# Kernel optimization log

Measured on AMD Instinct MI355X. Metric: run time of the kernel, lower is better.

Reference implementation:

```python
import jax, jax.numpy as jnp
import numpy as np

B, T, D, H, O = 64, 2048, 256, 256, 256


def setup_inputs() -> dict:
    key = jax.random.key(0)
    ks = jax.random.split(key, 4)
    s_d = float(1.0 / np.sqrt(D))
    s_h = float(1.0 / np.sqrt(H))
    return {
        "x": jax.random.normal(ks[0], (B, T, D), jnp.float32),
        "c0": jnp.zeros((B, H), jnp.float32),
        "h0": jnp.zeros((B, H), jnp.float32),
        "Wih": jax.random.normal(ks[1], (D, 4 * H), jnp.float32) * s_d,
        "Whh": jax.random.normal(ks[2], (H, 4 * H), jnp.float32) * s_h,
        "bh": jnp.zeros((4 * H,), jnp.float32),
        "Wout": jax.random.normal(ks[3], (H, O), jnp.float32) * s_h,
        "bout": jnp.zeros((O,), jnp.float32),
    }


def reference(x, c0, h0, Wih, Whh, bh, Wout, bout):
    # Teacher-forcing OneToManyRNN: LSTM cell + Dense projection each step.
    # Gate order (flax LSTMCell): i, f, g, o.
    def step(carry, xt):
        c, h = carry
        gates = xt @ Wih + h @ Whh + bh  # [B, 4H]
        i, f, g, o = jnp.split(gates, 4, axis=-1)
        i = jax.nn.sigmoid(i)
        f = jax.nn.sigmoid(f)
        g = jnp.tanh(g)
        o = jax.nn.sigmoid(o)
        c_new = f * c + i * g
        h_new = o * jnp.tanh(c_new)
        y = h_new @ Wout + bout  # dense_out projection
        return (c_new, h_new), y

    xs = jnp.swapaxes(x, 0, 1)  # [T, B, D]
    _, ys = jax.lax.scan(step, (c0, h0), xs)
    return jnp.swapaxes(ys, 0, 1)  # [B, T, O] (stacked per-step outputs)
```

## Files before the change

### kernel.cpp

```cpp
#include <hip/hip_runtime.h>
#include <hip/hip_fp16.h>
#include <cstdint>
#include <cstddef>

typedef _Float16 half_t;
typedef _Float16 half2_t __attribute__((ext_vector_type(2)));
typedef _Float16 half8_t __attribute__((ext_vector_type(8)));
typedef float    f32x4   __attribute__((ext_vector_type(4)));

#define T_FULL  2048
#define T_CH    512
#define N_CHUNK 4
#define B_SZ    64
#define H_SZ    256
#define G4      1024
#define CH_M    (B_SZ * T_CH)

#define KP_RF   48
#define KP_LDS  7
#define KP_STR  9

static constexpr size_t OFF_XW   = 0;
static constexpr size_t OFF_H    = OFF_XW   + (size_t)CH_M * G4 * 2;
static constexpr size_t OFF_WIH  = OFF_H    + (size_t)CH_M * H_SZ * 2;
static constexpr size_t OFF_WOUT = OFF_WIH  + (size_t)G4 * 256 * 2;
static constexpr size_t OFF_WRF  = OFF_WOUT + (size_t)256 * 256 * 2;
static constexpr size_t OFF_WLDS = OFF_WRF  + (size_t)2 * KP_RF * 1024 * 4;
static constexpr size_t OFF_WSTR = OFF_WLDS + (size_t)2 * KP_LDS * 256 * 16;
static constexpr size_t OFF_SC   = OFF_WSTR + (size_t)2 * KP_STR * 256 * 16;
static constexpr size_t OFF_SH   = OFF_SC   + (size_t)B_SZ * H_SZ * 4;

__device__ __forceinline__ unsigned int packh2(float a, float b) {
    half2_t h; h.x = (half_t)a; h.y = (half_t)b;
    return __builtin_bit_cast(unsigned int, h);
}

__device__ __forceinline__ float dot2f(unsigned int hp, unsigned int wp, float acc) {
#if __has_builtin(__builtin_amdgcn_fdot2)
    return __builtin_amdgcn_fdot2(__builtin_bit_cast(half2_t, hp),
                                  __builtin_bit_cast(half2_t, wp), acc, false);
#else
    half2_t h = __builtin_bit_cast(half2_t, hp);
    half2_t w = __builtin_bit_cast(half2_t, wp);
    return fmaf((float)h.y, (float)w.y, fmaf((float)h.x, (float)w.x, acc));
#endif
}

__device__ __forceinline__ unsigned int rlane(unsigned int v, int lane) {
    return (unsigned int)__builtin_amdgcn_readlane((int)v, lane);
}

__device__ __forceinline__ float sigm(float x)  { return 1.0f / (1.0f + __expf(-x)); }
__device__ __forceinline__ float tanh_(float x) { return 1.0f - 2.0f / (__expf(2.0f * x) + 1.0f); }

static constexpr int PACK_TOTAL = 262144 + 65536 + 2 * KP_RF * 1024
                                + 2 * KP_LDS * 256 * 4 + 2 * KP_STR * 256 * 4
                                + 16384 + 8192;

__global__ __launch_bounds__(256) void pack_kernel(
    const float* __restrict__ Wih, const float* __restrict__ Whh,
    const float* __restrict__ Wout, const float* __restrict__ c0,
    const float* __restrict__ h0,
    half_t* __restrict__ wih_t, half_t* __restrict__ wout_t,
    unsigned int* __restrict__ whh_rf, unsigned int* __restrict__ whh_lds,
    unsigned int* __restrict__ whh_str,
    float* __restrict__ state_c, unsigned int* __restrict__ state_h)
{
    const int stride = gridDim.x * blockDim.x;
    for (int idx = blockIdx.x * blockDim.x + threadIdx.x; idx < PACK_TOTAL; idx += stride) {
        int r = idx;
        if (r < 262144) {
            int n = r >> 8, k = r & 255;
            wih_t[r] = (half_t)Wih[k * 1024 + n];
            continue;
        }
        r -= 262144;
        if (r < 65536) {
            int n = r >> 8, k = r & 255;
            wout_t[r] = (half_t)Wout[k * 256 + n];
            continue;
        }
        r -= 65536;
        if (r < 2 * KP_RF * 1024) {
            int col = r & 1023, q2 = r >> 10;
            int hh = q2 / KP_RF, pl = q2 % KP_RF;
            int k0 = 2 * (hh * 64 + pl);
            whh_rf[r] = packh2(Whh[k0 * 1024 + col], Whh[(k0 + 1) * 1024 + col]);
            continue;
        }
        r -= 2 * KP_RF * 1024;
        if (r < 2 * KP_LDS * 256 * 4) {
            int j = r & 3, e = (r >> 2) & 255, rest = r >> 10;
            int ql = rest % KP_LDS, hh = rest / KP_LDS;
            int k0 = 2 * (hh * 64 + KP_RF + ql);
            int col = j * 256 + e;
            whh_lds[r] = packh2(Whh[k0 * 1024 + col], Whh[(k0 + 1) * 1024 + col]);
            continue;
        }
        r -= 2 * KP_LDS * 256 * 4;
        if (r < 2 * KP_STR * 256 * 4) {
            int j = r & 3, e = (r >> 2) & 255, rest = r >> 10;
            int sl = rest % KP_STR, hh = rest / KP_STR;
            int k0 = 2 * (hh * 64 + KP_RF + KP_LDS + sl);
            int col = j * 256 + e;
            whh_str[r] = packh2(Whh[k0 * 1024 + col], Whh[(k0 + 1) * 1024 + col]);
            continue;
        }
        r -= 2 * KP_STR * 256 * 4;
        if (r < 16384) { state_c[r] = c0[r]; continue; }
        r -= 16384;
        state_h[r] = packh2(h0[2 * r], h0[2 * r + 1]);
    }
}

template<int AMODE, int CMODE>
__global__ __launch_bounds__(256) void gemm16(
    const void* __restrict__ Ap, const half_t* __restrict__ Bt,
    void* __restrict__ Cp, const float* __restrict__ bias, int chunk0)
{
    __shared__ half_t Als[128][40];
    __shared__ half_t Bls[128][40];
    const int tid  = threadIdx.x;
    const int lane = tid & 63, wid = tid >> 6;
    const int wr = wid >> 1, wc = wid & 1;
    const int m0 = blockIdx.x * 128, n0 = blockIdx.y * 128;

    f32x4 acc[4][4] = {};

    for (int kc = 0; kc < 8; ++kc) {
        __syncthreads();
        if (AMODE == 1) {
            const float* A = (const float*)Ap;
            #pragma unroll
            for (int i = 0; i < 4; ++i) {
                int l = tid + i * 256;
                int row = l >> 3, kq = l & 7;
                int m = m0 + row;
                int arow = ((m >> 9) << 11) + chunk0 + (m & 511);
                f32x4 v = *(const f32x4*)(A + (size_t)arow * 256 + kc * 32 + kq * 4);
                uint2 pk;
                pk.x = packh2(v.x, v.y);
                pk.y = packh2(v.z, v.w);
                *reinterpret_cast<uint2*>(&Als[row][kq * 4]) = pk;
            }
        } else {
            const half_t* A = (const half_t*)Ap;
            #pragma unroll
            for (int i = 0; i < 2; ++i) {
                int l = tid + i * 256;
                int row = l >> 2, ko = l & 3;
                half8_t v = *(const half8_t*)(A + (size_t)(m0 + row) * 256 + kc * 32 + ko * 8);
                *reinterpret_cast<half8_t*>(&Als[row][ko * 8]) = v;
            }
        }
        #pragma unroll
        for (int i = 0; i < 2; ++i) {
            int l = tid + i * 256;
            int row = l >> 2, ko = l & 3;
            half8_t v = *(const half8_t*)(Bt + (size_t)(n0 + row) * 256 + kc * 32 + ko * 8);
            *reinterpret_cast<half8_t*>(&Bls[row][ko * 8]) = v;
        }
        __syncthreads();

        half8_t af[4], bf[4];
        #pragma unroll
        for (int mi = 0; mi < 4; ++mi)
            af[mi] = *reinterpret_cast<const half8_t*>(&Als[wr * 64 + mi * 16 + (lane & 15)][(lane >> 4) * 8]);
        #pragma unroll
        for (int ni = 0; ni < 4; ++ni)
            bf[ni] = *reinterpret_cast<const half8_t*>(&Bls[wc * 64 + ni * 16 + (lane & 15)][(lane >> 4) * 8]);
        #pragma unroll
        for (int mi = 0; mi < 4; ++mi)
            #pragma unroll
            for (int ni = 0; ni < 4; ++ni)
                acc[mi][ni] = __builtin_amdgcn_mfma_f32_16x16x32_f16(af[mi], bf[ni], acc[mi][ni], 0, 0, 0);
    }

    #pragma unroll
    for (int mi = 0; mi < 4; ++mi) {
        #pragma unroll
        for (int ni = 0; ni < 4; ++ni) {
            #pragma unroll
            for (int reg = 0; reg < 4; ++reg) {
                int row = m0 + wr * 64 + mi * 16 + (lane >> 4) * 4 + reg;
                int col = n0 + wc * 64 + ni * 16 + (lane & 15);
                float v = acc[mi][ni][reg] + bias[col];
                if (CMODE == 0) {
                    ((half_t*)Cp)[(size_t)row * 1024 + ((col & 255) << 2) + (col >> 8)] = (half_t)v;
                } else {
                    int crow = ((row >> 9) << 11) + chunk0 + (row & 511);
                    ((float*)Cp)[(size_t)crow * 256 + col] = v;
                }
            }
        }
    }
}

__global__ __launch_bounds__(512, 2) void rnn_kernel(
    const unsigned int* __restrict__ whh_rf,
    const uint4* __restrict__ whh_lds,
    const uint4* __restrict__ whh_str,
    const half_t* __restrict__ xw,
    half_t* __restrict__ h_out,
    float* __restrict__ state_c,
    unsigned int* __restrict__ state_h)
{
    __shared__ uint4  lds_w[2 * KP_LDS * 256];
    __shared__ float4 gbuf[256];
    __shared__ unsigned int hbuf[128];

    const int t    = threadIdx.x;
    const int e    = t & 255;
    const int hh   = t >> 8;
    const int lane = t & 63;
    const int b    = blockIdx.x;

    for (int i = t; i < 2 * KP_LDS * 256; i += 512) lds_w[i] = whh_lds[i];
    if (t < 128) hbuf[t] = state_h[b * 128 + t];
    float c = (hh == 0) ? state_c[b * 256 + e] : 0.0f;

    unsigned int wreg[KP_RF][4];
    {
        const unsigned int* wrp = whh_rf + hh * (KP_RF * 1024) + e;
        #pragma unroll
        for (int pl = 0; pl < KP_RF; ++pl)
            #pragma unroll
            for (int j = 0; j < 4; ++j)
                wreg[pl][j] = wrp[pl * 1024 + j * 256];
    }
    __syncthreads();

    const half_t* xwp = xw + (size_t)b * T_CH * 1024 + e * 4;
    half_t* hop = h_out + (size_t)b * T_CH * 256 + e;
    const uint4* strp = whh_str + hh * (KP_STR * 256) + e;
    const uint4* ldp  = lds_w + hh * (KP_LDS * 256) + e;

    for (int step = 0; step < T_CH; ++step) {
        unsigned int hv = hbuf[hh * 64 + lane];

        uint2 xv = {0, 0};
        if (hh == 0) xv = *(const uint2*)xwp;
        uint4 sq[KP_STR];
        #pragma unroll
        for (int sl = 0; sl < KP_STR; ++sl) sq[sl] = strp[sl * 256];

        float a0 = 0.f, a1 = 0.f, a2 = 0.f, a3 = 0.f;

        #pragma unroll
        for (int pl = 0; pl < KP_RF; ++pl) {
            unsigned int s = rlane(hv, pl);
            a0 = dot2f(s, wreg[pl][0], a0);
            a1 = dot2f(s, wreg[pl][1], a1);
            a2 = dot2f(s, wreg[pl][2], a2);
            a3 = dot2f(s, wreg[pl][3], a3);
        }
        #pragma unroll
        for (int sl = 0; sl < KP_STR; ++sl) {
            unsigned int s = rlane(hv, KP_RF + KP_LDS + sl);
            a0 = dot2f(s, sq[sl].x, a0);
            a1 = dot2f(s, sq[sl].y, a1);
            a2 = dot2f(s, sq[sl].z, a2);
            a3 = dot2f(s, sq[sl].w, a3);
        }
        #pragma unroll
        for (int ql = 0; ql < KP_LDS; ++ql) {
            uint4 q = ldp[ql * 256];
            unsigned int s = rlane(hv, KP_RF + ql);
            a0 = dot2f(s, q.x, a0);
            a1 = dot2f(s, q.y, a1);
            a2 = dot2f(s, q.z, a2);
            a3 = dot2f(s, q.w, a3);
        }

        if (hh) {
            float4 p; p.x = a0; p.y = a1; p.z = a2; p.w = a3;
            gbuf[e] = p;
        }
        __syncthreads();

        if (hh == 0) {
            float4 p = gbuf[e];
            half2_t x0 = __builtin_bit_cast(half2_t, xv.x);
            half2_t x1 = __builtin_bit_cast(half2_t, xv.y);
            a0 += p.x + (float)x0.x;
            a1 += p.y + (float)x0.y;
            a2 += p.z + (float)x1.x;
            a3 += p.w + (float)x1.y;
            float ig = sigm(a0), fg = sigm(a1), gg = tanh_(a2), og = sigm(a3);
            c = fg * c + ig * gg;
            float hn = og * tanh_(c);
            half_t h16 = (half_t)hn;
            reinterpret_cast<half_t*>(hbuf)[e] = h16;
            *hop = h16;
        }
        xwp += 1024;
        hop += 256;
        __syncthreads();
    }

    if (hh == 0) state_c[b * 256 + e] = c;
    if (t < 128) state_h[b * 128 + t] = hbuf[t];
}

extern "C" void kernel_launch(void* const* d_in, const int* in_sizes, int n_in,
                              void* d_out, int out_size, void* d_ws, size_t ws_size,
                              hipStream_t stream) {
    const float* x    = (const float*)d_in[0];
    const float* c0   = (const float*)d_in[1];
    const float* h0   = (const float*)d_in[2];
    const float* Wih  = (const float*)d_in[3];
    const float* Whh  = (const float*)d_in[4];
    const float* bh   = (const float*)d_in[5];
    const float* Wout = (const float*)d_in[6];
    const float* bout = (const float*)d_in[7];

    char* ws = (char*)d_ws;
    half_t* xw             = (half_t*)(ws + OFF_XW);
    half_t* h_chunk        = (half_t*)(ws + OFF_H);
    half_t* wih_t          = (half_t*)(ws + OFF_WIH);
    half_t* wout_t         = (half_t*)(ws + OFF_WOUT);
    unsigned int* whh_rf   = (unsigned int*)(ws + OFF_WRF);
    unsigned int* whh_lds  = (unsigned int*)(ws + OFF_WLDS);
    unsigned int* whh_str  = (unsigned int*)(ws + OFF_WSTR);
    float* state_c         = (float*)(ws + OFF_SC);
    unsigned int* state_h  = (unsigned int*)(ws + OFF_SH);

    pack_kernel<<<512, 256, 0, stream>>>(Wih, Whh, Wout, c0, h0,
                                         wih_t, wout_t, whh_rf, whh_lds, whh_str,
                                         state_c, state_h);

    for (int ch = 0; ch < N_CHUNK; ++ch) {
        int chunk0 = ch * T_CH;
        gemm16<1, 0><<<dim3(CH_M / 128, G4 / 128), 256, 0, stream>>>(
            (const void*)x, wih_t, (void*)xw, bh, chunk0);
        rnn_kernel<<<B_SZ, 512, 0, stream>>>(whh_rf, (const uint4*)whh_lds,
                                             (const uint4*)whh_str, xw, h_chunk,
                                             state_c, state_h);
        gemm16<0, 1><<<dim3(CH_M / 128, H_SZ / 128), 256, 0, stream>>>(
            (const void*)h_chunk, wout_t, d_out, bout, chunk0);
    }
    (void)in_sizes; (void)n_in; (void)out_size; (void)ws_size;
}
```

Baseline: 4.092 ms.

## Rebalance Whh split toward LDS, pin register weights, interleave loads with dots

Moves two k-pairs of the recurrent weights from per-step global streaming to LDS and repacks the register-resident weights as 16-byte vectors held in named variables pinned with empty asm, so the compiler keeps them in VGPRs. The step loop is split into two halves, each issuing its global and LDS loads before the register-weight dot products to hide load latency. The h output store moves after the second barrier. It adds LDS usage and depends on the compiler honouring the register pinning without spilling.

```diff
diff --git a/kernel.cpp b/kernel.cpp
--- a/kernel.cpp
+++ b/kernel.cpp
@@ -7,6 +7,7 @@
 typedef _Float16 half2_t __attribute__((ext_vector_type(2)));
 typedef _Float16 half8_t __attribute__((ext_vector_type(8)));
 typedef float    f32x4   __attribute__((ext_vector_type(4)));
+typedef unsigned int uint4v __attribute__((ext_vector_type(4)));
 
 #define T_FULL  2048
 #define T_CH    512
@@ -17,15 +18,15 @@
 #define CH_M    (B_SZ * T_CH)
 
 #define KP_RF   48
-#define KP_LDS  7
-#define KP_STR  9
+#define KP_LDS  9
+#define KP_STR  7
 
 static constexpr size_t OFF_XW   = 0;
 static constexpr size_t OFF_H    = OFF_XW   + (size_t)CH_M * G4 * 2;
 static constexpr size_t OFF_WIH  = OFF_H    + (size_t)CH_M * H_SZ * 2;
 static constexpr size_t OFF_WOUT = OFF_WIH  + (size_t)G4 * 256 * 2;
 static constexpr size_t OFF_WRF  = OFF_WOUT + (size_t)256 * 256 * 2;
-static constexpr size_t OFF_WLDS = OFF_WRF  + (size_t)2 * KP_RF * 1024 * 4;
+static constexpr size_t OFF_WLDS = OFF_WRF  + (size_t)2 * KP_RF * 256 * 16;
 static constexpr size_t OFF_WSTR = OFF_WLDS + (size_t)2 * KP_LDS * 256 * 16;
 static constexpr size_t OFF_SC   = OFF_WSTR + (size_t)2 * KP_STR * 256 * 16;
 static constexpr size_t OFF_SH   = OFF_SC   + (size_t)B_SZ * H_SZ * 4;
@@ -53,8 +54,10 @@
 __device__ __forceinline__ float sigm(float x)  { return 1.0f / (1.0f + __expf(-x)); }
 __device__ __forceinline__ float tanh_(float x) { return 1.0f - 2.0f / (__expf(2.0f * x) + 1.0f); }
 
-static constexpr int PACK_TOTAL = 262144 + 65536 + 2 * KP_RF * 1024
-                                + 2 * KP_LDS * 256 * 4 + 2 * KP_STR * 256 * 4
+static constexpr int PACK_TOTAL = 262144 + 65536
+                                + 2 * KP_RF  * 256 * 4
+                                + 2 * KP_LDS * 256 * 4
+                                + 2 * KP_STR * 256 * 4
                                 + 16384 + 8192;
 
 __global__ __launch_bounds__(256) void pack_kernel(
@@ -81,17 +84,18 @@
             continue;
         }
         r -= 65536;
-        if (r < 2 * KP_RF * 1024) {
-            int col = r & 1023, q2 = r >> 10;
-            int hh = q2 / KP_RF, pl = q2 % KP_RF;
+        if (r < 2 * KP_RF * 256 * 4) {
+            int j = r & 3, e = (r >> 2) & 255, q = r >> 10;
+            int pl = q % KP_RF, hh = q / KP_RF;
             int k0 = 2 * (hh * 64 + pl);
+            int col = j * 256 + e;
             whh_rf[r] = packh2(Whh[k0 * 1024 + col], Whh[(k0 + 1) * 1024 + col]);
             continue;
         }
-        r -= 2 * KP_RF * 1024;
+        r -= 2 * KP_RF * 256 * 4;
         if (r < 2 * KP_LDS * 256 * 4) {
-            int j = r & 3, e = (r >> 2) & 255, rest = r >> 10;
-            int ql = rest % KP_LDS, hh = rest / KP_LDS;
+            int j = r & 3, e = (r >> 2) & 255, q = r >> 10;
+            int ql = q % KP_LDS, hh = q / KP_LDS;
             int k0 = 2 * (hh * 64 + KP_RF + ql);
             int col = j * 256 + e;
             whh_lds[r] = packh2(Whh[k0 * 1024 + col], Whh[(k0 + 1) * 1024 + col]);
@@ -99,8 +103,8 @@
         }
         r -= 2 * KP_LDS * 256 * 4;
         if (r < 2 * KP_STR * 256 * 4) {
-            int j = r & 3, e = (r >> 2) & 255, rest = r >> 10;
-            int sl = rest % KP_STR, hh = rest / KP_STR;
+            int j = r & 3, e = (r >> 2) & 255, q = r >> 10;
+            int sl = q % KP_STR, hh = q / KP_STR;
             int k0 = 2 * (hh * 64 + KP_RF + KP_LDS + sl);
             int col = j * 256 + e;
             whh_str[r] = packh2(Whh[k0 * 1024 + col], Whh[(k0 + 1) * 1024 + col]);
@@ -196,17 +200,35 @@
     }
 }
 
+#define W_A(F) F(0) F(1) F(2) F(3) F(4) F(5) F(6) F(7) F(8) F(9) F(10) F(11) \
+               F(12) F(13) F(14) F(15) F(16) F(17) F(18) F(19) F(20) F(21) F(22) F(23)
+#define W_B(F) F(24) F(25) F(26) F(27) F(28) F(29) F(30) F(31) F(32) F(33) F(34) F(35) \
+               F(36) F(37) F(38) F(39) F(40) F(41) F(42) F(43) F(44) F(45) F(46) F(47)
+#define W_ALL(F) W_A(F) W_B(F)
+
+#define LDW(i)  uint4v w##i = wq[(i) * 256];
+#define PINW(i) asm volatile("" : "+v"(w##i));
+#define DOTW(i) { unsigned int s = rlane(hv, (i)); \
+    a0 = dot2f(s, w##i.x, a0); a1 = dot2f(s, w##i.y, a1); \
+    a2 = dot2f(s, w##i.z, a2); a3 = dot2f(s, w##i.w, a3); }
+#define DOTQ(i, q) { unsigned int s = rlane(hv, KP_RF + (i)); \
+    a0 = dot2f(s, (q).x, a0); a1 = dot2f(s, (q).y, a1); \
+    a2 = dot2f(s, (q).z, a2); a3 = dot2f(s, (q).w, a3); }
+#define DOTS(i, q) { unsigned int s = rlane(hv, KP_RF + KP_LDS + (i)); \
+    a0 = dot2f(s, (q).x, a0); a1 = dot2f(s, (q).y, a1); \
+    a2 = dot2f(s, (q).z, a2); a3 = dot2f(s, (q).w, a3); }
+
 __global__ __launch_bounds__(512, 2) void rnn_kernel(
-    const unsigned int* __restrict__ whh_rf,
-    const uint4* __restrict__ whh_lds,
-    const uint4* __restrict__ whh_str,
+    const uint4v* __restrict__ whh_rf,
+    const uint4v* __restrict__ whh_ldsrc,
+    const uint4v* __restrict__ whh_str,
     const half_t* __restrict__ xw,
     half_t* __restrict__ h_out,
     float* __restrict__ state_c,
     unsigned int* __restrict__ state_h)
 {
-    __shared__ uint4  lds_w[2 * KP_LDS * 256];
-    __shared__ float4 gbuf[256];
+    __shared__ uint4v lds_w[2 * KP_LDS * 256];
+    __shared__ f32x4  gbuf[256];
     __shared__ unsigned int hbuf[128];
 
     const int t    = threadIdx.x;
@@ -215,87 +237,75 @@
     const int lane = t & 63;
     const int b    = blockIdx.x;
 
-    for (int i = t; i < 2 * KP_LDS * 256; i += 512) lds_w[i] = whh_lds[i];
+    for (int i = t; i < 2 * KP_LDS * 256; i += 512) lds_w[i] = whh_ldsrc[i];
     if (t < 128) hbuf[t] = state_h[b * 128 + t];
     float c = (hh == 0) ? state_c[b * 256 + e] : 0.0f;
 
-    unsigned int wreg[KP_RF][4];
-    {
-        const unsigned int* wrp = whh_rf + hh * (KP_RF * 1024) + e;
-        #pragma unroll
-        for (int pl = 0; pl < KP_RF; ++pl)
-            #pragma unroll
-            for (int j = 0; j < 4; ++j)
-                wreg[pl][j] = wrp[pl * 1024 + j * 256];
-    }
+    const uint4v* wq = whh_rf + (size_t)hh * (KP_RF * 256) + e;
+    W_ALL(LDW)
+    W_ALL(PINW)
     __syncthreads();
 
     const half_t* xwp = xw + (size_t)b * T_CH * 1024 + e * 4;
     half_t* hop = h_out + (size_t)b * T_CH * 256 + e;
-    const uint4* strp = whh_str + hh * (KP_STR * 256) + e;
-    const uint4* ldp  = lds_w + hh * (KP_LDS * 256) + e;
+    const uint4v* strp = whh_str + hh * (KP_STR * 256) + e;
+    const uint4v* ldp  = lds_w + hh * (KP_LDS * 256) + e;
 
     for (int step = 0; step < T_CH; ++step) {
         unsigned int hv = hbuf[hh * 64 + lane];
 
-        uint2 xv = {0, 0};
+        uint2 xv; xv.x = 0; xv.y = 0;
         if (hh == 0) xv = *(const uint2*)xwp;
-        uint4 sq[KP_STR];
-        #pragma unroll
-        for (int sl = 0; sl < KP_STR; ++sl) sq[sl] = strp[sl * 256];
 
         float a0 = 0.f, a1 = 0.f, a2 = 0.f, a3 = 0.f;
 
-        #pragma unroll
-        for (int pl = 0; pl < KP_RF; ++pl) {
-            unsigned int s = rlane(hv, pl);
-            a0 = dot2f(s, wreg[pl][0], a0);
-            a1 = dot2f(s, wreg[pl][1], a1);
-            a2 = dot2f(s, wreg[pl][2], a2);
-            a3 = dot2f(s, wreg[pl][3], a3);
-        }
-        #pragma unroll
-        for (int sl = 0; sl < KP_STR; ++sl) {
-            unsigned int s = rlane(hv, KP_RF + KP_LDS + sl);
-            a0 = dot2f(s, sq[sl].x, a0);
-            a1 = dot2f(s, sq[sl].y, a1);
-            a2 = dot2f(s, sq[sl].z, a2);
-            a3 = dot2f(s, sq[sl].w, a3);
-        }
-        #pragma unroll
-        for (int ql = 0; ql < KP_LDS; ++ql) {
-            uint4 q = ldp[ql * 256];
-            unsigned int s = rlane(hv, KP_RF + ql);
-            a0 = dot2f(s, q.x, a0);
-            a1 = dot2f(s, q.y, a1);
-            a2 = dot2f(s, q.z, a2);
-            a3 = dot2f(s, q.w, a3);
+        {
+            uint4v t0 = strp[0],   t1 = strp[256],  t2 = strp[512],  t3 = strp[768];
+            uint4v q0 = ldp[0],    q1 = ldp[256],   q2 = ldp[512],   q3 = ldp[768];
+
+            W_A(DOTW)
+
+            DOTQ(0, q0) DOTQ(1, q1) DOTQ(2, q2) DOTQ(3, q3)
+            DOTS(0, t0) DOTS(1, t1) DOTS(2, t2) DOTS(3, t3)
+        }
+
+        {
+            uint4v t4 = strp[1024], t5 = strp[1280], t6 = strp[1536];
+            uint4v q4 = ldp[1024],  q5 = ldp[1280],  q6 = ldp[1536], q7 = ldp[1792];
+            uint4v q8 = ldp[2048];
+
+            W_B(DOTW)
+
+            DOTQ(4, q4) DOTQ(5, q5) DOTQ(6, q6) DOTQ(7, q7) DOTQ(8, q8)
+            DOTS(4, t4) DOTS(5, t5) DOTS(6, t6)
         }
 
         if (hh) {
-            float4 p; p.x = a0; p.y = a1; p.z = a2; p.w = a3;
+            f32x4 p; p[0] = a0; p[1] = a1; p[2] = a2; p[3] = a3;
             gbuf[e] = p;
         }
         __syncthreads();
 
+        half_t h16 = (half_t)0.f;
         if (hh == 0) {
-            float4 p = gbuf[e];
+            f32x4 p = gbuf[e];
             half2_t x0 = __builtin_bit_cast(half2_t, xv.x);
             half2_t x1 = __builtin_bit_cast(half2_t, xv.y);
-            a0 += p.x + (float)x0.x;
-            a1 += p.y + (float)x0.y;
-            a2 += p.z + (float)x1.x;
-            a3 += p.w + (float)x1.y;
+            a0 += p[0] + (float)x0.x;
+            a1 += p[1] + (float)x0.y;
+            a2 += p[2] + (float)x1.x;
+            a3 += p[3] + (float)x1.y;
             float ig = sigm(a0), fg = sigm(a1), gg = tanh_(a2), og = sigm(a3);
             c = fg * c + ig * gg;
             float hn = og * tanh_(c);
-            half_t h16 = (half_t)hn;
+            h16 = (half_t)hn;
             reinterpret_cast<half_t*>(hbuf)[e] = h16;
-            *hop = h16;
         }
         xwp += 1024;
+        __syncthreads();
+
+        if (hh == 0) *hop = h16;
         hop += 256;
-        __syncthreads();
     }
 
     if (hh == 0) state_c[b * 256 + e] = c;
@@ -333,9 +343,10 @@
         int chunk0 = ch * T_CH;
         gemm16<1, 0><<<dim3(CH_M / 128, G4 / 128), 256, 0, stream>>>(
             (const void*)x, wih_t, (void*)xw, bh, chunk0);
-        rnn_kernel<<<B_SZ, 512, 0, stream>>>(whh_rf, (const uint4*)whh_lds,
-                                             (const uint4*)whh_str, xw, h_chunk,
-                                             state_c, state_h);
+        rnn_kernel<<<B_SZ, 512, 0, stream>>>((const uint4v*)(ws + OFF_WRF),
+                                             (const uint4v*)(ws + OFF_WLDS),
+                                             (const uint4v*)(ws + OFF_WSTR),
+                                             xw, h_chunk, state_c, state_h);
         gemm16<0, 1><<<dim3(CH_M / 128, H_SZ / 128), 256, 0, stream>>>(
             (const void*)h_chunk, wout_t, d_out, bout, chunk0);
     }
```

After: 4.158 ms. Within noise of the previous version (+1.6%).

## Compute recurrent Whh matvec with MFMA instead of fdot2 readlane broadcast

Applied to the files above, without the earlier changes.

Replaces the per-thread fdot2 recurrent matvec, which broadcast h with readlane, with 16x16x32 f16 MFMA instructions. Only row 0 of the A operand is non-zero, so most of each MFMA's work is discarded. Whh is repacked into an MFMA B-fragment layout and split three ways: half the K tiles stay resident in registers, a quarter sit in LDS, and a quarter are reloaded from global/L2 every step. The aim is to cut the VALU and readlane cost per timestep. In exchange it wastes most of the MFMA throughput, adds per-step global loads, and adds an extra barrier before the h store.

```diff
diff --git a/kernel.cpp b/kernel.cpp
--- a/kernel.cpp
+++ b/kernel.cpp
@@ -7,6 +7,7 @@
 typedef _Float16 half2_t __attribute__((ext_vector_type(2)));
 typedef _Float16 half8_t __attribute__((ext_vector_type(8)));
 typedef float    f32x4   __attribute__((ext_vector_type(4)));
+typedef unsigned int uint4v __attribute__((ext_vector_type(4)));
 
 #define T_FULL  2048
 #define T_CH    512
@@ -16,18 +17,12 @@
 #define G4      1024
 #define CH_M    (B_SZ * T_CH)
 
-#define KP_RF   48
-#define KP_LDS  7
-#define KP_STR  9
-
 static constexpr size_t OFF_XW   = 0;
 static constexpr size_t OFF_H    = OFF_XW   + (size_t)CH_M * G4 * 2;
 static constexpr size_t OFF_WIH  = OFF_H    + (size_t)CH_M * H_SZ * 2;
 static constexpr size_t OFF_WOUT = OFF_WIH  + (size_t)G4 * 256 * 2;
-static constexpr size_t OFF_WRF  = OFF_WOUT + (size_t)256 * 256 * 2;
-static constexpr size_t OFF_WLDS = OFF_WRF  + (size_t)2 * KP_RF * 1024 * 4;
-static constexpr size_t OFF_WSTR = OFF_WLDS + (size_t)2 * KP_LDS * 256 * 16;
-static constexpr size_t OFF_SC   = OFF_WSTR + (size_t)2 * KP_STR * 256 * 16;
+static constexpr size_t OFF_WMF  = OFF_WOUT + (size_t)256 * 256 * 2;
+static constexpr size_t OFF_SC   = OFF_WMF  + (size_t)8 * 64 * 64 * 16;
 static constexpr size_t OFF_SH   = OFF_SC   + (size_t)B_SZ * H_SZ * 4;
 
 __device__ __forceinline__ unsigned int packh2(float a, float b) {
@@ -35,35 +30,17 @@
     return __builtin_bit_cast(unsigned int, h);
 }
 
-__device__ __forceinline__ float dot2f(unsigned int hp, unsigned int wp, float acc) {
-#if __has_builtin(__builtin_amdgcn_fdot2)
-    return __builtin_amdgcn_fdot2(__builtin_bit_cast(half2_t, hp),
-                                  __builtin_bit_cast(half2_t, wp), acc, false);
-#else
-    half2_t h = __builtin_bit_cast(half2_t, hp);
-    half2_t w = __builtin_bit_cast(half2_t, wp);
-    return fmaf((float)h.y, (float)w.y, fmaf((float)h.x, (float)w.x, acc));
-#endif
-}
-
-__device__ __forceinline__ unsigned int rlane(unsigned int v, int lane) {
-    return (unsigned int)__builtin_amdgcn_readlane((int)v, lane);
-}
-
 __device__ __forceinline__ float sigm(float x)  { return 1.0f / (1.0f + __expf(-x)); }
 __device__ __forceinline__ float tanh_(float x) { return 1.0f - 2.0f / (__expf(2.0f * x) + 1.0f); }
 
-static constexpr int PACK_TOTAL = 262144 + 65536 + 2 * KP_RF * 1024
-                                + 2 * KP_LDS * 256 * 4 + 2 * KP_STR * 256 * 4
-                                + 16384 + 8192;
+static constexpr int PACK_TOTAL = 262144 + 65536 + 131072 + 16384 + 8192;
 
 __global__ __launch_bounds__(256) void pack_kernel(
     const float* __restrict__ Wih, const float* __restrict__ Whh,
     const float* __restrict__ Wout, const float* __restrict__ c0,
     const float* __restrict__ h0,
     half_t* __restrict__ wih_t, half_t* __restrict__ wout_t,
-    unsigned int* __restrict__ whh_rf, unsigned int* __restrict__ whh_lds,
-    unsigned int* __restrict__ whh_str,
+    unsigned int* __restrict__ whh_mf,
     float* __restrict__ state_c, unsigned int* __restrict__ state_h)
 {
     const int stride = gridDim.x * blockDim.x;
@@ -81,32 +58,17 @@
             continue;
         }
         r -= 65536;
-        if (r < 2 * KP_RF * 1024) {
-            int col = r & 1023, q2 = r >> 10;
-            int hh = q2 / KP_RF, pl = q2 % KP_RF;
-            int k0 = 2 * (hh * 64 + pl);
-            whh_rf[r] = packh2(Whh[k0 * 1024 + col], Whh[(k0 + 1) * 1024 + col]);
+        if (r < 131072) {
+            int j    = r & 3;
+            int lane = (r >> 2) & 63;
+            int nt   = (r >> 8) & 63;
+            int kt   = r >> 14;
+            int k0 = kt * 32 + ((lane >> 4) << 3) + 2 * j;
+            int n  = nt * 16 + (lane & 15);
+            whh_mf[r] = packh2(Whh[k0 * 1024 + n], Whh[(k0 + 1) * 1024 + n]);
             continue;
         }
-        r -= 2 * KP_RF * 1024;
-        if (r < 2 * KP_LDS * 256 * 4) {
-            int j = r & 3, e = (r >> 2) & 255, rest = r >> 10;
-            int ql = rest % KP_LDS, hh = rest / KP_LDS;
-            int k0 = 2 * (hh * 64 + KP_RF + ql);
-            int col = j * 256 + e;
-            whh_lds[r] = packh2(Whh[k0 * 1024 + col], Whh[(k0 + 1) * 1024 + col]);
-            continue;
-        }
-        r -= 2 * KP_LDS * 256 * 4;
-        if (r < 2 * KP_STR * 256 * 4) {
-            int j = r & 3, e = (r >> 2) & 255, rest = r >> 10;
-            int sl = rest % KP_STR, hh = rest / KP_STR;
-            int k0 = 2 * (hh * 64 + KP_RF + KP_LDS + sl);
-            int col = j * 256 + e;
-            whh_str[r] = packh2(Whh[k0 * 1024 + col], Whh[(k0 + 1) * 1024 + col]);
-            continue;
-        }
-        r -= 2 * KP_STR * 256 * 4;
+        r -= 131072;
         if (r < 16384) { state_c[r] = c0[r]; continue; }
         r -= 16384;
         state_h[r] = packh2(h0[2 * r], h0[2 * r + 1]);
@@ -196,109 +158,96 @@
     }
 }
 
-__global__ __launch_bounds__(512, 2) void rnn_kernel(
-    const unsigned int* __restrict__ whh_rf,
-    const uint4* __restrict__ whh_lds,
-    const uint4* __restrict__ whh_str,
+__global__ __launch_bounds__(512) void rnn_kernel(
+    const uint4v* __restrict__ whh_mf,
     const half_t* __restrict__ xw,
     half_t* __restrict__ h_out,
     float* __restrict__ state_c,
     unsigned int* __restrict__ state_h)
 {
-    __shared__ uint4  lds_w[2 * KP_LDS * 256];
-    __shared__ float4 gbuf[256];
+    __shared__ uint4v lds_b[2 * 4096];
+    __shared__ float  gbuf[1024];
     __shared__ unsigned int hbuf[128];
 
     const int t    = threadIdx.x;
+    const int lane = t & 63;
+    const int w    = t >> 6;
     const int e    = t & 255;
-    const int hh   = t >> 8;
-    const int lane = t & 63;
     const int b    = blockIdx.x;
 
-    for (int i = t; i < 2 * KP_LDS * 256; i += 512) lds_w[i] = whh_lds[i];
+    for (int i = t; i < 8192; i += 512) lds_b[i] = whh_mf[4 * 4096 + i];
     if (t < 128) hbuf[t] = state_h[b * 128 + t];
-    float c = (hh == 0) ? state_c[b * 256 + e] : 0.0f;
-
-    unsigned int wreg[KP_RF][4];
-    {
-        const unsigned int* wrp = whh_rf + hh * (KP_RF * 1024) + e;
-        #pragma unroll
-        for (int pl = 0; pl < KP_RF; ++pl)
-            #pragma unroll
-            for (int j = 0; j < 4; ++j)
-                wreg[pl][j] = wrp[pl * 1024 + j * 256];
-    }
+    float c = (t < 256) ? state_c[b * 256 + e] : 0.0f;
+
+    const half8_t* mf8 = (const half8_t*)whh_mf;
+    half8_t Bres[4][8];
+    #pragma unroll
+    for (int r = 0; r < 4; ++r)
+        #pragma unroll
+        for (int ntl = 0; ntl < 8; ++ntl)
+            Bres[r][ntl] = mf8[(r * 64 + w * 8 + ntl) * 64 + lane];
     __syncthreads();
 
     const half_t* xwp = xw + (size_t)b * T_CH * 1024 + e * 4;
     half_t* hop = h_out + (size_t)b * T_CH * 256 + e;
-    const uint4* strp = whh_str + hh * (KP_STR * 256) + e;
-    const uint4* ldp  = lds_w + hh * (KP_LDS * 256) + e;
-
+    const half_t* hbh = (const half_t*)hbuf;
+
+    #pragma unroll 1
     for (int step = 0; step < T_CH; ++step) {
-        unsigned int hv = hbuf[hh * 64 + lane];
-
-        uint2 xv = {0, 0};
-        if (hh == 0) xv = *(const uint2*)xwp;
-        uint4 sq[KP_STR];
-        #pragma unroll
-        for (int sl = 0; sl < KP_STR; ++sl) sq[sl] = strp[sl * 256];
-
-        float a0 = 0.f, a1 = 0.f, a2 = 0.f, a3 = 0.f;
-
-        #pragma unroll
-        for (int pl = 0; pl < KP_RF; ++pl) {
-            unsigned int s = rlane(hv, pl);
-            a0 = dot2f(s, wreg[pl][0], a0);
-            a1 = dot2f(s, wreg[pl][1], a1);
-            a2 = dot2f(s, wreg[pl][2], a2);
-            a3 = dot2f(s, wreg[pl][3], a3);
-        }
-        #pragma unroll
-        for (int sl = 0; sl < KP_STR; ++sl) {
-            unsigned int s = rlane(hv, KP_RF + KP_LDS + sl);
-            a0 = dot2f(s, sq[sl].x, a0);
-            a1 = dot2f(s, sq[sl].y, a1);
-            a2 = dot2f(s, sq[sl].z, a2);
-            a3 = dot2f(s, sq[sl].w, a3);
-        }
-        #pragma unroll
-        for (int ql = 0; ql < KP_LDS; ++ql) {
-            uint4 q = ldp[ql * 256];
-            unsigned int s = rlane(hv, KP_RF + ql);
-            a0 = dot2f(s, q.x, a0);
-            a1 = dot2f(s, q.y, a1);
-            a2 = dot2f(s, q.z, a2);
-            a3 = dot2f(s, q.w, a3);
-        }
-
-        if (hh) {
-            float4 p; p.x = a0; p.y = a1; p.z = a2; p.w = a3;
-            gbuf[e] = p;
-        }
-        __syncthreads();
-
-        if (hh == 0) {
-            float4 p = gbuf[e];
+        uint2 xv; xv.x = 0; xv.y = 0;
+        if (t < 256) xv = *(const uint2*)xwp;
+
+        half8_t a[8];
+        #pragma unroll
+        for (int kt = 0; kt < 8; ++kt) {
+            half8_t v = {};
+            if ((lane & 15) == 0)
+                v = *(const half8_t*)(hbh + kt * 32 + (lane >> 4) * 8);
+            a[kt] = v;
+        }
+
+        #pragma unroll
+        for (int ntl = 0; ntl < 8; ++ntl) {
+            const int nt = w * 8 + ntl;
+            half8_t l4 = *(const half8_t*)&lds_b[0 * 4096 + nt * 64 + lane];
+            half8_t l5 = *(const half8_t*)&lds_b[1 * 4096 + nt * 64 + lane];
+            half8_t g6 = mf8[(6 * 64 + nt) * 64 + lane];
+            half8_t g7 = mf8[(7 * 64 + nt) * 64 + lane];
+            f32x4 cc = {};
+            cc = __builtin_amdgcn_mfma_f32_16x16x32_f16(a[0], Bres[0][ntl], cc, 0, 0, 0);
+            cc = __builtin_amdgcn_mfma_f32_16x16x32_f16(a[1], Bres[1][ntl], cc, 0, 0, 0);
+            cc = __builtin_amdgcn_mfma_f32_16x16x32_f16(a[2], Bres[2][ntl], cc, 0, 0, 0);
+            cc = __builtin_amdgcn_mfma_f32_16x16x32_f16(a[3], Bres[3][ntl], cc, 0, 0, 0);
+            cc = __builtin_amdgcn_mfma_f32_16x16x32_f16(a[4], l4, cc, 0, 0, 0);
+            cc = __builtin_amdgcn_mfma_f32_16x16x32_f16(a[5], l5, cc, 0, 0, 0);
+            cc = __builtin_amdgcn_mfma_f32_16x16x32_f16(a[6], g6, cc, 0, 0, 0);
+            cc = __builtin_amdgcn_mfma_f32_16x16x32_f16(a[7], g7, cc, 0, 0, 0);
+            if (lane < 16) gbuf[nt * 16 + lane] = cc[0];
+        }
+        __syncthreads();
+
+        half_t h16 = (half_t)0.f;
+        if (t < 256) {
             half2_t x0 = __builtin_bit_cast(half2_t, xv.x);
             half2_t x1 = __builtin_bit_cast(half2_t, xv.y);
-            a0 += p.x + (float)x0.x;
-            a1 += p.y + (float)x0.y;
-            a2 += p.z + (float)x1.x;
-            a3 += p.w + (float)x1.y;
+            float a0 = gbuf[e]       + (float)x0.x;
+            float a1 = gbuf[256 + e] + (float)x0.y;
+            float a2 = gbuf[512 + e] + (float)x1.x;
+            float a3 = gbuf[768 + e] + (float)x1.y;
             float ig = sigm(a0), fg = sigm(a1), gg = tanh_(a2), og = sigm(a3);
             c = fg * c + ig * gg;
             float hn = og * tanh_(c);
-            half_t h16 = (half_t)hn;
-            reinterpret_cast<half_t*>(hbuf)[e] = h16;
-            *hop = h16;
+            h16 = (half_t)hn;
+            ((half_t*)hbuf)[e] = h16;
         }
         xwp += 1024;
+        __syncthreads();
+
+        if (t < 256) *hop = h16;
         hop += 256;
-        __syncthreads();
-    }
-
-    if (hh == 0) state_c[b * 256 + e] = c;
+    }
+
+    if (t < 256) state_c[b * 256 + e] = c;
     if (t < 128) state_h[b * 128 + t] = hbuf[t];
 }
 
@@ -319,23 +268,20 @@
     half_t* h_chunk        = (half_t*)(ws + OFF_H);
     half_t* wih_t          = (half_t*)(ws + OFF_WIH);
     half_t* wout_t         = (half_t*)(ws + OFF_WOUT);
-    unsigned int* whh_rf   = (unsigned int*)(ws + OFF_WRF);
-    unsigned int* whh_lds  = (unsigned int*)(ws + OFF_WLDS);
-    unsigned int* whh_str  = (unsigned int*)(ws + OFF_WSTR);
+    unsigned int* whh_mf   = (unsigned int*)(ws + OFF_WMF);
     float* state_c         = (float*)(ws + OFF_SC);
     unsigned int* state_h  = (unsigned int*)(ws + OFF_SH);
 
     pack_kernel<<<512, 256, 0, stream>>>(Wih, Whh, Wout, c0, h0,
-                                         wih_t, wout_t, whh_rf, whh_lds, whh_str,
+                                         wih_t, wout_t, whh_mf,
                                          state_c, state_h);
 
     for (int ch = 0; ch < N_CHUNK; ++ch) {
         int chunk0 = ch * T_CH;
         gemm16<1, 0><<<dim3(CH_M / 128, G4 / 128), 256, 0, stream>>>(
             (const void*)x, wih_t, (void*)xw, bh, chunk0);
-        rnn_kernel<<<B_SZ, 512, 0, stream>>>(whh_rf, (const uint4*)whh_lds,
-                                             (const uint4*)whh_str, xw, h_chunk,
-                                             state_c, state_h);
+        rnn_kernel<<<B_SZ, 512, 0, stream>>>((const uint4v*)(ws + OFF_WMF),
+                                             xw, h_chunk, state_c, state_h);
         gemm16<0, 1><<<dim3(CH_M / 128, H_SZ / 128), 256, 0, stream>>>(
             (const void*)h_chunk, wout_t, d_out, bout, chunk0);
     }
```

After: 3.839 ms. -6.2%, faster.
